# Kernel tuning notes

Hardware: AMD Instinct MI355X
Metric: run time of the kernel (lower is better)

The kernel has to match this reference:

```python
import jax, jax.numpy as jnp
import numpy as np

B, N, C = 128, 196, 2048   # batch, regions (14x14), conv channels
H, A = 512, 512            # hidden_size, attention_size


def setup_inputs() -> dict:
    key = jax.random.key(0)
    ks = jax.random.split(key, 10)
    s = lambda d: 1.0 / np.sqrt(d)
    return {
        "img_embedding": jax.random.normal(ks[0], (B, N, C), jnp.float32),
        "hidden": jax.random.normal(ks[1], (B, H), jnp.float32),
        "W_img": jax.random.uniform(ks[2], (C, A), jnp.float32, -s(C), s(C)),
        "b_img": jax.random.uniform(ks[3], (A,), jnp.float32, -s(C), s(C)),
        "W_hid": jax.random.uniform(ks[4], (H, A), jnp.float32, -s(H), s(H)),
        "b_hid": jax.random.uniform(ks[5], (A,), jnp.float32, -s(H), s(H)),
        "w_att": jax.random.uniform(ks[6], (A,), jnp.float32, -s(A), s(A)),
        "b_att": jax.random.uniform(ks[7], (), jnp.float32, -s(A), s(A)),
        "w_beta": jax.random.uniform(ks[8], (H,), jnp.float32, -s(H), s(H)),
        "b_beta": jax.random.uniform(ks[9], (), jnp.float32, -s(H), s(H)),
    }


def reference(img_embedding, hidden, W_img, b_img, W_hid, b_hid,
              w_att, b_att, w_beta, b_beta):
    # img_embedding: (B, N, C); hidden: (B, H)
    img_att = jnp.einsum('bnc,ca->bna', img_embedding, W_img) + b_img   # (B,N,A)
    hid_att = hidden @ W_hid + b_hid                                    # (B,A)
    # additive attention scores -> (B, N)
    scores = jnp.einsum('bna,a->bn',
                        jax.nn.relu(img_att + hid_att[:, None, :]), w_att) + b_att
    beta = jax.nn.sigmoid(hidden @ w_beta + b_beta)                     # (B,)
    attention_weights = jax.nn.softmax(scores, axis=-1)                 # (B,N)
    context = beta[:, None] * jnp.einsum('bn,bnc->bc',
                                         attention_weights, img_embedding)  # (B,C)
    return context, attention_weights
```

## Files before the change

### kernel.cpp

```cpp
#include <hip/hip_runtime.h>
#include <hip/hip_bf16.h>
#include <math.h>

typedef __bf16 bf16v8 __attribute__((ext_vector_type(8)));
typedef __bf16 bf16v4 __attribute__((ext_vector_type(4)));
typedef float  f32x4  __attribute__((ext_vector_type(4)));

__device__ __forceinline__ void gload_lds16(const void* g, void* l) {
    __builtin_amdgcn_global_load_lds(
        (const __attribute__((address_space(1))) unsigned int*)g,
        (__attribute__((address_space(3))) unsigned int*)l, 16, 0, 0);
}

__device__ __forceinline__ void cvt_w4(void* dst, float4 a) {
    bf16v4 v;
    v[0] = (__bf16)a.x; v[1] = (__bf16)a.y;
    v[2] = (__bf16)a.z; v[3] = (__bf16)a.w;
    *(bf16v4*)dst = v;
}

__global__ __launch_bounds__(256) void wt_k(const float* __restrict__ W,
                                            unsigned short* __restrict__ Wt)
{
    __shared__ float tile[64][65];
    const int k0 = blockIdx.x * 64;
    const int a0 = blockIdx.y * 64;
    const int t = threadIdx.x;
    const int c = t & 63, rbase = t >> 6;
#pragma unroll
    for (int i = 0; i < 16; ++i) {
        int kr = rbase + i * 4;
        tile[kr][c] = W[(k0 + kr) * 512 + a0 + c];
    }
    __syncthreads();
#pragma unroll
    for (int i = 0; i < 16; ++i) {
        int ar = rbase + i * 4;
        Wt[(a0 + ar) * 2048 + k0 + c] =
            __builtin_bit_cast(unsigned short, (__bf16)tile[c][ar]);
    }
}

__global__ __launch_bounds__(256) void hid_k(
    const float* __restrict__ hidden, const float* __restrict__ W_hid,
    const float* __restrict__ b_hid,  const float* __restrict__ b_img,
    const float* __restrict__ w_beta, const float* __restrict__ b_beta,
    float* __restrict__ hb, float* __restrict__ betap)
{
    const int b = blockIdx.x, t = threadIdx.x;
    __shared__ float hs[512];
    __shared__ float red[4];
    hs[t]       = hidden[b * 512 + t];
    hs[t + 256] = hidden[b * 512 + 256 + t];
    __syncthreads();
    float a0 = 0.f, a1 = 0.f;
#pragma unroll 4
    for (int h = 0; h < 512; ++h) {
        float hv = hs[h];
        a0 = fmaf(hv, W_hid[h * 512 + t], a0);
        a1 = fmaf(hv, W_hid[h * 512 + 256 + t], a1);
    }
    hb[b * 512 + t]       = a0 + b_hid[t]       + b_img[t];
    hb[b * 512 + 256 + t] = a1 + b_hid[256 + t] + b_img[256 + t];

    float x = hs[t] * w_beta[t] + hs[t + 256] * w_beta[t + 256];
#pragma unroll
    for (int k = 32; k >= 1; k >>= 1) x += __shfl_xor(x, k, 64);
    const int lane = t & 63, wid = t >> 6;
    if (lane == 0) red[wid] = x;
    __syncthreads();
    if (t == 0) {
        float s = red[0] + red[1] + red[2] + red[3] + b_beta[0];
        betap[b] = 1.f / (1.f + __expf(-s));
    }
}

__global__ __launch_bounds__(256, 3) void scores_gemm(
    const float* __restrict__ img,
    const unsigned short* __restrict__ Wt,
    const float* __restrict__ hb,
    const float* __restrict__ w_att,
    float* __restrict__ partials)
{
    __shared__ __align__(16) char smem[36864];
    char* A0 = smem;
    char* A1 = smem + 10240;
    char* B0 = smem + 20480;
    char* B1 = smem + 28672;

    const int tid  = threadIdx.x;
    const int lane = tid & 63;
    const int wid  = tid >> 6;
    const int wm   = wid >> 1;
    const int wn   = wid & 1;

    const int id = blockIdx.x;
    const int wg = (id & 7) * 98 + (id >> 3);
    const int cb    = wg & 3;
    const int mtile = wg >> 2;
    const int r0 = mtile * 128;
    const int a0 = cb * 128;

    const int ar = tid >> 2;
    const int ac = (tid & 3) * 4;
    const float* gA0 = img + (size_t)(r0 + ar) * 2048 + ac;
    const float* gA1 = img + (size_t)(r0 + 64 + ar) * 2048 + ac;
    const int aW0 = ar * 80 + ac * 2;
    const int aW1 = (64 + ar) * 80 + ac * 2;

    const int bswz = ((tid & 3) ^ ((tid >> 3) & 3)) * 8;
    const unsigned short* gB0 = Wt + (size_t)(a0 + (tid >> 2)) * 2048 + bswz;
    const unsigned short* gB1 = Wt + (size_t)(a0 + 64 + (tid >> 2)) * 2048 + bswz;
    const int bW0 = tid * 16;
    const int bW1 = 4096 + tid * 16;

    const int g  = lane >> 4;
    const int fl = lane & 15;
    const int bro = (g ^ ((fl >> 1) & 3)) << 4;

    f32x4 acc[4][4] = {};
    float4 rA0[4], rA1[4];

#define ALOAD(RC, IT) do {                                                   \
    RC[0] = *(const float4*)(gA0 + (IT) * 32);                               \
    RC[1] = *(const float4*)(gA0 + (IT) * 32 + 16);                          \
    RC[2] = *(const float4*)(gA1 + (IT) * 32);                               \
    RC[3] = *(const float4*)(gA1 + (IT) * 32 + 16);                          \
} while (0)

#define ACVT(DST, RC) do {                                                   \
    cvt_w4(DST + aW0,      RC[0]);                                           \
    cvt_w4(DST + aW0 + 32, RC[1]);                                           \
    cvt_w4(DST + aW1,      RC[2]);                                           \
    cvt_w4(DST + aW1 + 32, RC[3]);                                           \
} while (0)

    ALOAD(rA0, 0);
    gload_lds16(gB0, B0 + bW0);
    gload_lds16(gB1, B0 + bW1);
    __builtin_amdgcn_sched_barrier(0);
    ACVT(A0, rA0);
    ALOAD(rA0, 1);
    ALOAD(rA1, 2);
    __syncthreads();

#define BODY(K, CA, CB, NA, NB, RC, STAGE, RELOAD, FULLBAR) do {             \
    bf16v8 av[4], bv[4];                                                     \
    _Pragma("unroll")                                                        \
    for (int fm = 0; fm < 4; ++fm) {                                         \
        int row = wm * 64 + fm * 16 + fl;                                    \
        av[fm] = *(const bf16v8*)(CA + row * 80 + g * 16);                   \
    }                                                                        \
    _Pragma("unroll")                                                        \
    for (int fn = 0; fn < 4; ++fn) {                                         \
        int col = wn * 64 + fn * 16 + fl;                                    \
        bv[fn] = *(const bf16v8*)(CB + col * 64 + bro);                      \
    }                                                                        \
    if (STAGE) {                                                             \
        gload_lds16(gB0 + (K + 1) * 32, NB + bW0);                           \
        gload_lds16(gB1 + (K + 1) * 32, NB + bW1);                           \
    }                                                                        \
    __builtin_amdgcn_sched_barrier(0);                                       \
    if (STAGE) ACVT(NA, RC);                                                 \
    if (RELOAD) ALOAD(RC, K + 3);                                            \
    __builtin_amdgcn_sched_barrier(0);                                       \
    _Pragma("unroll")                                                        \
    for (int fm = 0; fm < 4; ++fm)                                           \
        _Pragma("unroll")                                                    \
        for (int fn = 0; fn < 4; ++fn)                                       \
            acc[fm][fn] = __builtin_amdgcn_mfma_f32_16x16x32_bf16(           \
                av[fm], bv[fn], acc[fm][fn], 0, 0, 0);                       \
    if (FULLBAR) {                                                           \
        __syncthreads();                                                     \
    } else {                                                                 \
        __builtin_amdgcn_sched_barrier(0);                                   \
        asm volatile("s_waitcnt vmcnt(4) lgkmcnt(0)" ::: "memory");          \
        __builtin_amdgcn_s_barrier();                                        \
        __builtin_amdgcn_sched_barrier(0);                                   \
    }                                                                        \
} while (0)

    for (int t = 0; t < 60; t += 2) {
        BODY(t,     A0, B0, A1, B1, rA0, true, true, false);
        BODY(t + 1, A1, B1, A0, B0, rA1, true, true, false);
    }
    BODY(60, A0, B0, A1, B1, rA0, true,  true,  false);
    BODY(61, A1, B1, A0, B0, rA1, true,  false, true);
    BODY(62, A0, B0, A1, B1, rA0, true,  false, true);
    BODY(63, A1, B1, A0, B0, rA1, false, false, true);
#undef BODY
#undef ALOAD
#undef ACVT

    float* red = (float*)smem;
    const int l4 = lane >> 4;

    float w4[4];
#pragma unroll
    for (int fn = 0; fn < 4; ++fn) w4[fn] = w_att[a0 + wn * 64 + fn * 16 + fl];

#pragma unroll
    for (int fm = 0; fm < 4; ++fm) {
#pragma unroll
        for (int rg = 0; rg < 4; ++rg) {
            int row = wm * 64 + fm * 16 + l4 * 4 + rg;
            int grow = r0 + row;
            int bb = grow / 196;
            const float* hbrow = hb + bb * 512 + a0 + wn * 64;
            float s = 0.f;
#pragma unroll
            for (int fn = 0; fn < 4; ++fn) {
                float v = acc[fm][fn][rg] + hbrow[fn * 16 + fl];
                v = fmaxf(v, 0.f);
                s = fmaf(v, w4[fn], s);
            }
#pragma unroll
            for (int m = 1; m < 16; m <<= 1) s += __shfl_xor(s, m, 64);
            if (fl == 0) red[wn * 128 + row] = s;
        }
    }
    __syncthreads();
    if (tid < 128) {
        partials[cb * 25088 + r0 + tid] = red[tid] + red[128 + tid];
    }
}

__global__ __launch_bounds__(256) void softmax_k(
    const float* __restrict__ partials, const float* __restrict__ betap,
    const float* __restrict__ b_att,
    float* __restrict__ out_w, float* __restrict__ wbeta)
{
    const int b = blockIdx.x;
    const int t = threadIdx.x;
    const int lane = t & 63, wid = t >> 6;
    __shared__ float red[4];

    float scv = 0.f, sc = -1e30f;
    if (t < 196) {
        int r = b * 196 + t;
        scv = partials[r] + partials[25088 + r] + partials[2 * 25088 + r] +
              partials[3 * 25088 + r] + b_att[0];
        sc = scv;
    }
    float m = sc;
#pragma unroll
    for (int k = 32; k >= 1; k >>= 1) m = fmaxf(m, __shfl_xor(m, k, 64));
    if (lane == 0) red[wid] = m;
    __syncthreads();
    m = fmaxf(fmaxf(red[0], red[1]), fmaxf(red[2], red[3]));

    float e = (t < 196) ? __expf(scv - m) : 0.f;
    float ssum = e;
#pragma unroll
    for (int k = 32; k >= 1; k >>= 1) ssum += __shfl_xor(ssum, k, 64);
    __syncthreads();
    if (lane == 0) red[wid] = ssum;
    __syncthreads();
    float denom = red[0] + red[1] + red[2] + red[3];

    if (t < 196) {
        float w = e / denom;
        out_w[b * 196 + t] = w;
        wbeta[b * 196 + t] = w * betap[b];
    }
}

__global__ __launch_bounds__(256) void ctx_k(
    const float* __restrict__ img, const float* __restrict__ wbeta,
    float* __restrict__ out)
{
    const int b = blockIdx.y;
    const int c0 = blockIdx.x * 512 + threadIdx.x * 2;
    __shared__ float w[200];
    if (threadIdx.x < 196) w[threadIdx.x] = wbeta[b * 196 + threadIdx.x];
    __syncthreads();
    const float* base = img + (size_t)b * 196 * 2048 + c0;
    float acx = 0.f, acy = 0.f;
#pragma unroll 4
    for (int n = 0; n < 196; ++n) {
        float2 v = *(const float2*)(base + (size_t)n * 2048);
        float wn = w[n];
        acx = fmaf(wn, v.x, acx);
        acy = fmaf(wn, v.y, acy);
    }
    float2 r; r.x = acx; r.y = acy;
    *(float2*)(out + b * 2048 + c0) = r;
}

extern "C" void kernel_launch(void* const* d_in, const int* in_sizes, int n_in,
                              void* d_out, int out_size, void* d_ws, size_t ws_size,
                              hipStream_t stream)
{
    const float* img    = (const float*)d_in[0];
    const float* hidden = (const float*)d_in[1];
    const float* W_img  = (const float*)d_in[2];
    const float* b_img  = (const float*)d_in[3];
    const float* W_hid  = (const float*)d_in[4];
    const float* b_hid  = (const float*)d_in[5];
    const float* w_att  = (const float*)d_in[6];
    const float* b_att  = (const float*)d_in[7];
    const float* w_beta = (const float*)d_in[8];
    const float* b_beta = (const float*)d_in[9];

    char* ws = (char*)d_ws;
    unsigned short* Wt = (unsigned short*)ws;
    float* hbp   = (float*)(ws + 2097152);
    float* betap = (float*)(ws + 2359296);
    float* parts = (float*)(ws + 2359808);
    float* wbeta = (float*)(ws + 2761216);

    float* out_ctx = (float*)d_out;
    float* out_w   = out_ctx + 128 * 2048;

    wt_k<<<dim3(32, 8), 256, 0, stream>>>(W_img, Wt);
    hid_k<<<128, 256, 0, stream>>>(hidden, W_hid, b_hid, b_img, w_beta, b_beta,
                                   hbp, betap);
    scores_gemm<<<784, 256, 0, stream>>>(img, Wt, hbp, w_att, parts);
    softmax_k<<<128, 256, 0, stream>>>(parts, betap, b_att, out_w, wbeta);
    ctx_k<<<dim3(4, 128), 256, 0, stream>>>(img, wbeta, out_ctx);
}
```

Baseline: 210.9 us.

## Process two K-steps per barrier with four-stage LDS buffers in scores GEMM

Restructures the scores GEMM main loop so that each barrier covers two K-steps. It uses four A and four B LDS buffers (64 KB) instead of two padded double buffers. Each thread now converts eight contiguous fp32 values into one 16-byte bf16 LDS store, and the A row stride drops from 80 to 64 bytes. The aim is to halve the number of barriers per K and to use wider LDS writes. In exchange, occupancy drops from 3 to 2 blocks per CU, more registers hold prefetched data, and the unpadded A layout may cause LDS bank conflicts on the fragment reads.

```diff
diff --git a/kernel.cpp b/kernel.cpp
--- a/kernel.cpp
+++ b/kernel.cpp
@@ -3,7 +3,6 @@
 #include <math.h>
 
 typedef __bf16 bf16v8 __attribute__((ext_vector_type(8)));
-typedef __bf16 bf16v4 __attribute__((ext_vector_type(4)));
 typedef float  f32x4  __attribute__((ext_vector_type(4)));
 
 __device__ __forceinline__ void gload_lds16(const void* g, void* l) {
@@ -12,11 +11,11 @@
         (__attribute__((address_space(3))) unsigned int*)l, 16, 0, 0);
 }
 
-__device__ __forceinline__ void cvt_w4(void* dst, float4 a) {
-    bf16v4 v;
-    v[0] = (__bf16)a.x; v[1] = (__bf16)a.y;
-    v[2] = (__bf16)a.z; v[3] = (__bf16)a.w;
-    *(bf16v4*)dst = v;
+__device__ __forceinline__ void cvt_store8(void* dst, float4 a, float4 b) {
+    bf16v8 v;
+    v[0] = (__bf16)a.x; v[1] = (__bf16)a.y; v[2] = (__bf16)a.z; v[3] = (__bf16)a.w;
+    v[4] = (__bf16)b.x; v[5] = (__bf16)b.y; v[6] = (__bf16)b.z; v[7] = (__bf16)b.w;
+    *(bf16v8*)dst = v;
 }
 
 __global__ __launch_bounds__(256) void wt_k(const float* __restrict__ W,
@@ -75,18 +74,22 @@
     }
 }
 
-__global__ __launch_bounds__(256, 3) void scores_gemm(
+__global__ __launch_bounds__(256, 2) void scores_gemm(
     const float* __restrict__ img,
     const unsigned short* __restrict__ Wt,
     const float* __restrict__ hb,
     const float* __restrict__ w_att,
     float* __restrict__ partials)
 {
-    __shared__ __align__(16) char smem[36864];
+    __shared__ __align__(16) char smem[65536];
     char* A0 = smem;
-    char* A1 = smem + 10240;
-    char* B0 = smem + 20480;
-    char* B1 = smem + 28672;
+    char* A1 = smem + 8192;
+    char* A2 = smem + 16384;
+    char* A3 = smem + 24576;
+    char* B0 = smem + 32768;
+    char* B1 = smem + 40960;
+    char* B2 = smem + 49152;
+    char* B3 = smem + 57344;
 
     const int tid  = threadIdx.x;
     const int lane = tid & 63;
@@ -102,11 +105,11 @@
     const int a0 = cb * 128;
 
     const int ar = tid >> 2;
-    const int ac = (tid & 3) * 4;
-    const float* gA0 = img + (size_t)(r0 + ar) * 2048 + ac;
-    const float* gA1 = img + (size_t)(r0 + 64 + ar) * 2048 + ac;
-    const int aW0 = ar * 80 + ac * 2;
-    const int aW1 = (64 + ar) * 80 + ac * 2;
+    const int aq = tid & 3;
+    const float* gA0 = img + (size_t)(r0 + ar) * 2048 + aq * 8;
+    const float* gA1 = img + (size_t)(r0 + 64 + ar) * 2048 + aq * 8;
+    const int aW0 = ar * 64 + aq * 16;
+    const int aW1 = (64 + ar) * 64 + aq * 16;
 
     const int bswz = ((tid & 3) ^ ((tid >> 3) & 3)) * 8;
     const unsigned short* gB0 = Wt + (size_t)(a0 + (tid >> 2)) * 2048 + bswz;
@@ -121,76 +124,75 @@
     f32x4 acc[4][4] = {};
     float4 rA0[4], rA1[4];
 
-#define ALOAD(RC, IT) do {                                                   \
-    RC[0] = *(const float4*)(gA0 + (IT) * 32);                               \
-    RC[1] = *(const float4*)(gA0 + (IT) * 32 + 16);                          \
-    RC[2] = *(const float4*)(gA1 + (IT) * 32);                               \
-    RC[3] = *(const float4*)(gA1 + (IT) * 32 + 16);                          \
+#define ALOAD(RC, K) do {                                                    \
+    RC[0] = *(const float4*)(gA0 + (K) * 32);                                \
+    RC[1] = *(const float4*)(gA0 + (K) * 32 + 4);                            \
+    RC[2] = *(const float4*)(gA1 + (K) * 32);                                \
+    RC[3] = *(const float4*)(gA1 + (K) * 32 + 4);                            \
 } while (0)
 
 #define ACVT(DST, RC) do {                                                   \
-    cvt_w4(DST + aW0,      RC[0]);                                           \
-    cvt_w4(DST + aW0 + 32, RC[1]);                                           \
-    cvt_w4(DST + aW1,      RC[2]);                                           \
-    cvt_w4(DST + aW1 + 32, RC[3]);                                           \
+    cvt_store8(DST + aW0, RC[0], RC[1]);                                     \
+    cvt_store8(DST + aW1, RC[2], RC[3]);                                     \
 } while (0)
 
-    ALOAD(rA0, 0);
-    gload_lds16(gB0, B0 + bW0);
-    gload_lds16(gB1, B0 + bW1);
-    __builtin_amdgcn_sched_barrier(0);
-    ACVT(A0, rA0);
-    ALOAD(rA0, 1);
-    ALOAD(rA1, 2);
-    __syncthreads();
-
-#define BODY(K, CA, CB, NA, NB, RC, STAGE, RELOAD, FULLBAR) do {             \
+#define MSTEP(CA, CB) do {                                                   \
     bf16v8 av[4], bv[4];                                                     \
     _Pragma("unroll")                                                        \
-    for (int fm = 0; fm < 4; ++fm) {                                         \
-        int row = wm * 64 + fm * 16 + fl;                                    \
-        av[fm] = *(const bf16v8*)(CA + row * 80 + g * 16);                   \
-    }                                                                        \
+    for (int fm = 0; fm < 4; ++fm)                                           \
+        av[fm] = *(const bf16v8*)(CA + (wm * 64 + fm * 16 + fl) * 64 + g * 16);\
     _Pragma("unroll")                                                        \
-    for (int fn = 0; fn < 4; ++fn) {                                         \
-        int col = wn * 64 + fn * 16 + fl;                                    \
-        bv[fn] = *(const bf16v8*)(CB + col * 64 + bro);                      \
-    }                                                                        \
-    if (STAGE) {                                                             \
-        gload_lds16(gB0 + (K + 1) * 32, NB + bW0);                           \
-        gload_lds16(gB1 + (K + 1) * 32, NB + bW1);                           \
-    }                                                                        \
-    __builtin_amdgcn_sched_barrier(0);                                       \
-    if (STAGE) ACVT(NA, RC);                                                 \
-    if (RELOAD) ALOAD(RC, K + 3);                                            \
-    __builtin_amdgcn_sched_barrier(0);                                       \
+    for (int fn = 0; fn < 4; ++fn)                                           \
+        bv[fn] = *(const bf16v8*)(CB + (wn * 64 + fn * 16 + fl) * 64 + bro); \
     _Pragma("unroll")                                                        \
     for (int fm = 0; fm < 4; ++fm)                                           \
         _Pragma("unroll")                                                    \
         for (int fn = 0; fn < 4; ++fn)                                       \
             acc[fm][fn] = __builtin_amdgcn_mfma_f32_16x16x32_bf16(           \
                 av[fm], bv[fn], acc[fm][fn], 0, 0, 0);                       \
-    if (FULLBAR) {                                                           \
-        __syncthreads();                                                     \
-    } else {                                                                 \
-        __builtin_amdgcn_sched_barrier(0);                                   \
-        asm volatile("s_waitcnt vmcnt(4) lgkmcnt(0)" ::: "memory");          \
-        __builtin_amdgcn_s_barrier();                                        \
-        __builtin_amdgcn_sched_barrier(0);                                   \
+} while (0)
+
+#define BODYP(K, CA0, CB0, CA1, CB1, NA0, NB0, NA1, NB1, STAGE, RELOAD, SYNC)\
+do {                                                                         \
+    if (STAGE) {                                                             \
+        gload_lds16(gB0 + (K + 2) * 32, NB0 + bW0);                          \
+        gload_lds16(gB1 + (K + 2) * 32, NB0 + bW1);                          \
+        gload_lds16(gB0 + (K + 3) * 32, NB1 + bW0);                          \
+        gload_lds16(gB1 + (K + 3) * 32, NB1 + bW1);                          \
+        ACVT(NA0, rA0);                                                      \
+        ACVT(NA1, rA1);                                                      \
     }                                                                        \
+    if (RELOAD) {                                                            \
+        ALOAD(rA0, K + 4);                                                   \
+        ALOAD(rA1, K + 5);                                                   \
+    }                                                                        \
+    MSTEP(CA0, CB0);                                                         \
+    MSTEP(CA1, CB1);                                                         \
+    if (SYNC) __syncthreads();                                               \
 } while (0)
 
-    for (int t = 0; t < 60; t += 2) {
-        BODY(t,     A0, B0, A1, B1, rA0, true, true, false);
-        BODY(t + 1, A1, B1, A0, B0, rA1, true, true, false);
-    }
-    BODY(60, A0, B0, A1, B1, rA0, true,  true,  false);
-    BODY(61, A1, B1, A0, B0, rA1, true,  false, true);
-    BODY(62, A0, B0, A1, B1, rA0, true,  false, true);
-    BODY(63, A1, B1, A0, B0, rA1, false, false, true);
-#undef BODY
+    ALOAD(rA0, 0);
+    ALOAD(rA1, 1);
+    gload_lds16(gB0, B0 + bW0);
+    gload_lds16(gB1, B0 + bW1);
+    gload_lds16(gB0 + 32, B1 + bW0);
+    gload_lds16(gB1 + 32, B1 + bW1);
+    ACVT(A0, rA0);
+    ACVT(A1, rA1);
+    ALOAD(rA0, 2);
+    ALOAD(rA1, 3);
+    __syncthreads();
+
+    for (int k = 0; k < 60; k += 4) {
+        BODYP(k,     A0, B0, A1, B1, A2, B2, A3, B3, true, true, true);
+        BODYP(k + 2, A2, B2, A3, B3, A0, B0, A1, B1, true, true, true);
+    }
+    BODYP(60, A0, B0, A1, B1, A2, B2, A3, B3, true,  false, true);
+    BODYP(62, A2, B2, A3, B3, A0, B0, A1, B1, false, false, false);
+#undef BODYP
+#undef MSTEP
+#undef ACVT
 #undef ALOAD
-#undef ACVT
 
     float* red = (float*)smem;
     const int l4 = lane >> 4;
```

Measured after the change: 193.7 us. 8.1% less time.

## Retile scores GEMM to 64x256 tiles with 1x4 warp layout

Applied to the files above, without the earlier changes.

Changes the scores GEMM block tile from 128 rows x 128 attention columns to 64 rows x 256 columns. Each warp now covers all 64 rows and its own 64-column slice, and the A conversion stores 8 bf16 at once. The split over attention columns drops from four partial-score planes to two, so softmax sums fewer partials and each image row's fp32 data is loaded and converted by half as many blocks. The cost is more W traffic per block (four B stage loads), a larger LDS footprint, and a different waitcnt depth.

```diff
diff --git a/kernel.cpp b/kernel.cpp
--- a/kernel.cpp
+++ b/kernel.cpp
@@ -3,7 +3,6 @@
 #include <math.h>
 
 typedef __bf16 bf16v8 __attribute__((ext_vector_type(8)));
-typedef __bf16 bf16v4 __attribute__((ext_vector_type(4)));
 typedef float  f32x4  __attribute__((ext_vector_type(4)));
 
 __device__ __forceinline__ void gload_lds16(const void* g, void* l) {
@@ -12,11 +11,11 @@
         (__attribute__((address_space(3))) unsigned int*)l, 16, 0, 0);
 }
 
-__device__ __forceinline__ void cvt_w4(void* dst, float4 a) {
-    bf16v4 v;
-    v[0] = (__bf16)a.x; v[1] = (__bf16)a.y;
-    v[2] = (__bf16)a.z; v[3] = (__bf16)a.w;
-    *(bf16v4*)dst = v;
+__device__ __forceinline__ void cvt_store8(void* dst, float4 a, float4 b) {
+    bf16v8 v;
+    v[0] = (__bf16)a.x; v[1] = (__bf16)a.y; v[2] = (__bf16)a.z; v[3] = (__bf16)a.w;
+    v[4] = (__bf16)b.x; v[5] = (__bf16)b.y; v[6] = (__bf16)b.z; v[7] = (__bf16)b.w;
+    *(bf16v8*)dst = v;
 }
 
 __global__ __launch_bounds__(256) void wt_k(const float* __restrict__ W,
@@ -82,86 +81,75 @@
     const float* __restrict__ w_att,
     float* __restrict__ partials)
 {
-    __shared__ __align__(16) char smem[36864];
+    __shared__ __align__(16) char smem[40960];
     char* A0 = smem;
-    char* A1 = smem + 10240;
-    char* B0 = smem + 20480;
-    char* B1 = smem + 28672;
+    char* A1 = smem + 4096;
+    char* B0 = smem + 8192;
+    char* B1 = smem + 24576;
 
     const int tid  = threadIdx.x;
     const int lane = tid & 63;
     const int wid  = tid >> 6;
-    const int wm   = wid >> 1;
-    const int wn   = wid & 1;
 
     const int id = blockIdx.x;
     const int wg = (id & 7) * 98 + (id >> 3);
-    const int cb    = wg & 3;
-    const int mtile = wg >> 2;
-    const int r0 = mtile * 128;
-    const int a0 = cb * 128;
+    const int cb    = wg & 1;
+    const int mtile = wg >> 1;
+    const int r0 = mtile * 64;
+    const int a0 = cb * 256;
 
     const int ar = tid >> 2;
-    const int ac = (tid & 3) * 4;
-    const float* gA0 = img + (size_t)(r0 + ar) * 2048 + ac;
-    const float* gA1 = img + (size_t)(r0 + 64 + ar) * 2048 + ac;
-    const int aW0 = ar * 80 + ac * 2;
-    const int aW1 = (64 + ar) * 80 + ac * 2;
+    const int aq = tid & 3;
+    const float* gA = img + (size_t)(r0 + ar) * 2048 + aq * 8;
+    const int aW = ar * 64 + aq * 16;
 
     const int bswz = ((tid & 3) ^ ((tid >> 3) & 3)) * 8;
-    const unsigned short* gB0 = Wt + (size_t)(a0 + (tid >> 2)) * 2048 + bswz;
-    const unsigned short* gB1 = Wt + (size_t)(a0 + 64 + (tid >> 2)) * 2048 + bswz;
-    const int bW0 = tid * 16;
-    const int bW1 = 4096 + tid * 16;
+    const unsigned short* gBp0 = Wt + (size_t)(a0 + (tid >> 2)) * 2048 + bswz;
+    const unsigned short* gBp1 = gBp0 + (size_t)64 * 2048;
+    const unsigned short* gBp2 = gBp0 + (size_t)128 * 2048;
+    const unsigned short* gBp3 = gBp0 + (size_t)192 * 2048;
+    const int bW = tid * 16;
 
     const int g  = lane >> 4;
     const int fl = lane & 15;
     const int bro = (g ^ ((fl >> 1) & 3)) << 4;
 
     f32x4 acc[4][4] = {};
-    float4 rA0[4], rA1[4];
-
-#define ALOAD(RC, IT) do {                                                   \
-    RC[0] = *(const float4*)(gA0 + (IT) * 32);                               \
-    RC[1] = *(const float4*)(gA0 + (IT) * 32 + 16);                          \
-    RC[2] = *(const float4*)(gA1 + (IT) * 32);                               \
-    RC[3] = *(const float4*)(gA1 + (IT) * 32 + 16);                          \
+    float4 rA0[2], rA1[2];
+
+#define ALOAD(RC, K) do {                                                    \
+    RC[0] = *(const float4*)(gA + (K) * 32);                                 \
+    RC[1] = *(const float4*)(gA + (K) * 32 + 4);                             \
 } while (0)
 
-#define ACVT(DST, RC) do {                                                   \
-    cvt_w4(DST + aW0,      RC[0]);                                           \
-    cvt_w4(DST + aW0 + 32, RC[1]);                                           \
-    cvt_w4(DST + aW1,      RC[2]);                                           \
-    cvt_w4(DST + aW1 + 32, RC[3]);                                           \
+#define STAGEB(K, NB) do {                                                   \
+    gload_lds16(gBp0 + (K) * 32, NB + bW);                                   \
+    gload_lds16(gBp1 + (K) * 32, NB + 4096 + bW);                            \
+    gload_lds16(gBp2 + (K) * 32, NB + 8192 + bW);                            \
+    gload_lds16(gBp3 + (K) * 32, NB + 12288 + bW);                           \
 } while (0)
 
     ALOAD(rA0, 0);
-    gload_lds16(gB0, B0 + bW0);
-    gload_lds16(gB1, B0 + bW1);
+    STAGEB(0, B0);
     __builtin_amdgcn_sched_barrier(0);
-    ACVT(A0, rA0);
+    cvt_store8(A0 + aW, rA0[0], rA0[1]);
     ALOAD(rA0, 1);
     ALOAD(rA1, 2);
     __syncthreads();
 
-#define BODY(K, CA, CB, NA, NB, RC, STAGE, RELOAD, FULLBAR) do {             \
+#define BODY(K, CA, CB, NA, NB, RC, STAGE, DOCVT, RELOAD, BAR) do {          \
     bf16v8 av[4], bv[4];                                                     \
     _Pragma("unroll")                                                        \
-    for (int fm = 0; fm < 4; ++fm) {                                         \
-        int row = wm * 64 + fm * 16 + fl;                                    \
-        av[fm] = *(const bf16v8*)(CA + row * 80 + g * 16);                   \
-    }                                                                        \
+    for (int fm = 0; fm < 4; ++fm)                                           \
+        av[fm] = *(const bf16v8*)(CA + (fm * 16 + fl) * 64 + g * 16);        \
     _Pragma("unroll")                                                        \
     for (int fn = 0; fn < 4; ++fn) {                                         \
-        int col = wn * 64 + fn * 16 + fl;                                    \
+        int col = wid * 64 + fn * 16 + fl;                                   \
         bv[fn] = *(const bf16v8*)(CB + col * 64 + bro);                      \
     }                                                                        \
-    if (STAGE) {                                                             \
-        gload_lds16(gB0 + (K + 1) * 32, NB + bW0);                           \
-        gload_lds16(gB1 + (K + 1) * 32, NB + bW1);                           \
-    }                                                                        \
+    if (STAGE) STAGEB(K + 1, NB);                                            \
     __builtin_amdgcn_sched_barrier(0);                                       \
-    if (STAGE) ACVT(NA, RC);                                                 \
+    if (DOCVT) cvt_store8(NA + aW, RC[0], RC[1]);                            \
     if (RELOAD) ALOAD(RC, K + 3);                                            \
     __builtin_amdgcn_sched_barrier(0);                                       \
     _Pragma("unroll")                                                        \
@@ -170,43 +158,43 @@
         for (int fn = 0; fn < 4; ++fn)                                       \
             acc[fm][fn] = __builtin_amdgcn_mfma_f32_16x16x32_bf16(           \
                 av[fm], bv[fn], acc[fm][fn], 0, 0, 0);                       \
-    if (FULLBAR) {                                                           \
+    if (BAR == 1) {                                                          \
         __syncthreads();                                                     \
-    } else {                                                                 \
+    } else if (BAR == 0) {                                                   \
         __builtin_amdgcn_sched_barrier(0);                                   \
-        asm volatile("s_waitcnt vmcnt(4) lgkmcnt(0)" ::: "memory");          \
+        asm volatile("s_waitcnt vmcnt(2) lgkmcnt(0)" ::: "memory");          \
         __builtin_amdgcn_s_barrier();                                        \
         __builtin_amdgcn_sched_barrier(0);                                   \
     }                                                                        \
 } while (0)
 
     for (int t = 0; t < 60; t += 2) {
-        BODY(t,     A0, B0, A1, B1, rA0, true, true, false);
-        BODY(t + 1, A1, B1, A0, B0, rA1, true, true, false);
-    }
-    BODY(60, A0, B0, A1, B1, rA0, true,  true,  false);
-    BODY(61, A1, B1, A0, B0, rA1, true,  false, true);
-    BODY(62, A0, B0, A1, B1, rA0, true,  false, true);
-    BODY(63, A1, B1, A0, B0, rA1, false, false, true);
+        BODY(t,     A0, B0, A1, B1, rA0, true, true, true, 0);
+        BODY(t + 1, A1, B1, A0, B0, rA1, true, true, true, 0);
+    }
+    BODY(60, A0, B0, A1, B1, rA0, true,  true,  true,  0);
+    BODY(61, A1, B1, A0, B0, rA1, true,  true,  false, 1);
+    BODY(62, A0, B0, A1, B1, rA0, true,  true,  false, 1);
+    BODY(63, A1, B1, A0, B0, rA1, false, false, false, 2);
 #undef BODY
+#undef STAGEB
 #undef ALOAD
-#undef ACVT
 
     float* red = (float*)smem;
     const int l4 = lane >> 4;
 
     float w4[4];
 #pragma unroll
-    for (int fn = 0; fn < 4; ++fn) w4[fn] = w_att[a0 + wn * 64 + fn * 16 + fl];
+    for (int fn = 0; fn < 4; ++fn) w4[fn] = w_att[a0 + wid * 64 + fn * 16 + fl];
 
 #pragma unroll
     for (int fm = 0; fm < 4; ++fm) {
 #pragma unroll
         for (int rg = 0; rg < 4; ++rg) {
-            int row = wm * 64 + fm * 16 + l4 * 4 + rg;
+            int row = fm * 16 + l4 * 4 + rg;
             int grow = r0 + row;
             int bb = grow / 196;
-            const float* hbrow = hb + bb * 512 + a0 + wn * 64;
+            const float* hbrow = hb + bb * 512 + a0 + wid * 64;
             float s = 0.f;
 #pragma unroll
             for (int fn = 0; fn < 4; ++fn) {
@@ -216,12 +204,13 @@
             }
 #pragma unroll
             for (int m = 1; m < 16; m <<= 1) s += __shfl_xor(s, m, 64);
-            if (fl == 0) red[wn * 128 + row] = s;
+            if (fl == 0) red[wid * 64 + row] = s;
         }
     }
     __syncthreads();
-    if (tid < 128) {
-        partials[cb * 25088 + r0 + tid] = red[tid] + red[128 + tid];
+    if (tid < 64) {
+        partials[cb * 25088 + r0 + tid] =
+            red[tid] + red[64 + tid] + red[128 + tid] + red[192 + tid];
     }
 }
 
@@ -238,8 +227,7 @@
     float scv = 0.f, sc = -1e30f;
     if (t < 196) {
         int r = b * 196 + t;
-        scv = partials[r] + partials[25088 + r] + partials[2 * 25088 + r] +
-              partials[3 * 25088 + r] + b_att[0];
+        scv = partials[r] + partials[25088 + r] + b_att[0];
         sc = scv;
     }
     float m = sc;
```

New measurement: 202.1 us. -4.2%, faster.
